# Kernel tuning notes

Hardware: AMD Instinct MI355X
Metric: run time of the kernel (lower is better)

## Reference

```python
import jax, jax.numpy as jnp
import numpy as np

EMB = 768
HEADS = 8
HEAD_DIM = EMB // HEADS  # 96


def setup_inputs() -> dict:
    key = jax.random.key(0)
    k1, k2, k3, k4, k5 = jax.random.split(key, 5)
    N, S = 2, 4096
    values = jax.random.normal(k1, (N, S, EMB), dtype=jnp.float32)
    keys = jax.random.normal(k2, (N, S, EMB), dtype=jnp.float32)
    query = jax.random.normal(k3, (N, S, EMB), dtype=jnp.float32)
    # fc_out: nn.Linear(emb_size, emb_size) -> weight [out,in], bias [out]
    bound = 1.0 / np.sqrt(EMB)
    fc_w = jax.random.uniform(k4, (EMB, EMB), dtype=jnp.float32, minval=-bound, maxval=bound)
    fc_b = jax.random.uniform(k5, (EMB,), dtype=jnp.float32, minval=-bound, maxval=bound)
    return {"values": values, "keys": keys, "query": query, "fc_w": fc_w, "fc_b": fc_b}


def reference(values, keys, query, fc_w, fc_b):
    # NOTE: original forward never uses the per-head q/k/v Linear layers;
    # it reshapes raw inputs into heads directly. We reproduce that faithfully.
    N, Sq, _ = query.shape
    # [N, S, E] -> [N, H, S, D]
    q = query.reshape(N, Sq, HEADS, HEAD_DIM).transpose(0, 2, 1, 3)
    k = keys.reshape(N, -1, HEADS, HEAD_DIM).transpose(0, 2, 1, 3)
    v = values.reshape(N, -1, HEADS, HEAD_DIM).transpose(0, 2, 1, 3)
    scale = 1.0 / np.sqrt(HEAD_DIM).astype(np.float32)
    scores = jnp.einsum('nhqd,nhkd->nhqk', q, k) * scale  # [N,H,Sq,Sk]
    p = jax.nn.softmax(scores, axis=-1)
    x = jnp.einsum('nhqk,nhkd->nhqd', p, v)  # [N,H,Sq,D]
    x = x.transpose(0, 2, 1, 3).reshape(N, Sq, EMB)
    return x @ fc_w.T + fc_b
```

## Files before the change

kernel.cpp:

```cpp
#include <hip/hip_runtime.h>
#include <hip/hip_bf16.h>

#define S_LEN 4096
#define EMB 768
#define NHEAD 8
#define HDIM 96

typedef short bf16x8 __attribute__((ext_vector_type(8)));
typedef float f32x4 __attribute__((ext_vector_type(4)));
typedef float f32x16 __attribute__((ext_vector_type(16)));

__device__ __forceinline__ short f2bf(float x) {
  union { float f; unsigned u; } v; v.f = x;
  unsigned r = v.u + 0x7fffu + ((v.u >> 16) & 1u);
  return (short)(r >> 16);
}

__device__ __forceinline__ short f2bfh(float x) {
  union { __hip_bfloat16 h; short s; } u;
  u.h = __float2bfloat16(x);
  return u.s;
}

#define GLOAD_LDS16(gp, lp)                                              \
  __builtin_amdgcn_global_load_lds(                                      \
      (const __attribute__((address_space(1))) unsigned int*)(gp),       \
      (__attribute__((address_space(3))) unsigned int*)(lp), 16, 0, 0)

__global__ __launch_bounds__(256) void prep_kernel(const float* __restrict__ K,
                                                   const float* __restrict__ W,
                                                   const float* __restrict__ V,
                                                   short* __restrict__ KVT,
                                                   short* __restrict__ Wb) {
  __shared__ short tlbuf[6656];
  int b = blockIdx.x;
  int tid = threadIdx.x;
  if (b < 288) {
    int t = b * 256 + tid;
    size_t off = (size_t)t * 8;
    float4 a = *(const float4*)(W + off);
    float4 bq = *(const float4*)(W + off + 4);
    bf16x8 r;
    r[0]=f2bf(a.x);  r[1]=f2bf(a.y);  r[2]=f2bf(a.z);  r[3]=f2bf(a.w);
    r[4]=f2bf(bq.x); r[5]=f2bf(bq.y); r[6]=f2bf(bq.z); r[7]=f2bf(bq.w);
    *(bf16x8*)(Wb + off) = r;
    return;
  }
  if (b < 1312) {
    int bb = b - 288;
    int n = bb >> 9, h = (bb >> 6) & 7, st = bb & 63;
    int s0 = st * 64;
    const float* kp = K + ((size_t)(n * S_LEN + s0)) * EMB + h * HDIM;
    #pragma unroll
    for (int k = 0; k < 6; ++k) {
      int idx = k * 256 + tid;
      int fidx = idx * 4;
      int s = fidx / 96, d = fidx % 96;
      float4 a = *(const float4*)(kp + (size_t)s * EMB + d);
      short* t4 = &tlbuf[s * 104 + d];
      t4[0] = f2bf(a.x); t4[1] = f2bf(a.y); t4[2] = f2bf(a.z); t4[3] = f2bf(a.w);
    }
    __syncthreads();
    short* KVp = KVT + ((size_t)((n * NHEAD + h) * 64 + st)) * 12288;
    #pragma unroll
    for (int i = 0; i < 3; ++i) {
      int u = i * 256 + tid;
      int c = u >> 7, rem = u & 127;
      int ksub = (rem >> 6) & 1, hi2 = (rem >> 5) & 1, l31 = rem & 31;
      int key = ksub * 32 + l31;
      int db = c * 16 + hi2 * 8;
      short4 lo = *(const short4*)&tlbuf[key * 104 + db];
      short4 hi4 = *(const short4*)&tlbuf[key * 104 + db + 4];
      bf16x8 r;
      r[0]=lo.x; r[1]=lo.y; r[2]=lo.z; r[3]=lo.w;
      r[4]=hi4.x; r[5]=hi4.y; r[6]=hi4.z; r[7]=hi4.w;
      *(bf16x8*)(KVp + (size_t)u * 8) = r;
    }
    return;
  }
  int bb = b - 1312;
  int n = bb >> 9, h = (bb >> 6) & 7, st = bb & 63;
  int s0 = st * 64;
  const float* vp = V + ((size_t)(n * S_LEN + s0)) * EMB + h * HDIM;
  #pragma unroll
  for (int k = 0; k < 6; ++k) {
    int idx = k * 256 + tid;
    int fidx = idx * 4;
    int s = fidx / 96, d = fidx % 96;
    float4 a = *(const float4*)(vp + (size_t)s * EMB + d);
    tlbuf[(d + 0) * 68 + s] = f2bf(a.x);
    tlbuf[(d + 1) * 68 + s] = f2bf(a.y);
    tlbuf[(d + 2) * 68 + s] = f2bf(a.z);
    tlbuf[(d + 3) * 68 + s] = f2bf(a.w);
  }
  __syncthreads();
  short* KVp = KVT + ((size_t)((n * NHEAD + h) * 64 + st)) * 12288 + 6144;
  #pragma unroll
  for (int i = 0; i < 3; ++i) {
    int u = i * 256 + tid;
    int slice = u / 192;
    int rem = u - slice * 192;
    int dt = rem >> 6, hi2 = (rem >> 5) & 1, d5 = rem & 31;
    int d = dt * 32 + d5;
    int kb = 16 * slice + 4 * hi2;
    short4 lo = *(const short4*)&tlbuf[d * 68 + kb];
    short4 hi4 = *(const short4*)&tlbuf[d * 68 + kb + 8];
    bf16x8 r;
    r[0]=lo.x; r[1]=lo.y; r[2]=lo.z; r[3]=lo.w;
    r[4]=hi4.x; r[5]=hi4.y; r[6]=hi4.z; r[7]=hi4.w;
    *(bf16x8*)(KVp + (size_t)u * 8) = r;
  }
}

template<int NKG>
__global__ __launch_bounds__(128, 2) void attn_kernel(const float* __restrict__ Q,
                                                      const short* __restrict__ KVT,
                                                      short* __restrict__ Xb,
                                                      float* __restrict__ Op,
                                                      float* __restrict__ lp) {
  __shared__ __align__(16) char smem[36864];
  constexpr int ITERS = S_LEN / NKG / 64;
  int L = blockIdx.x;
  int bb = L & 511;
  int kg = L >> 9;
  int h = bb & 7, j = bb >> 3;
  int n = j >> 5, qt = j & 31;
  int q0 = qt * 128;
  int tid = threadIdx.x;
  int w = tid >> 6, lane = tid & 63, l31 = lane & 31, hi = lane >> 5;

  const float kAdj = 0.14724512f;
  bf16x8 qfa[6], qfb[6];
  #pragma unroll
  for (int sub = 0; sub < 2; ++sub) {
    const float* qp = Q + ((size_t)(n * S_LEN + q0 + w * 64 + sub * 32 + l31)) * EMB
                        + h * HDIM + 8 * hi;
    #pragma unroll
    for (int c = 0; c < 6; ++c) {
      float4 a = *(const float4*)(qp + 16 * c);
      float4 bq = *(const float4*)(qp + 16 * c + 4);
      bf16x8 r;
      r[0]=f2bf(a.x*kAdj);  r[1]=f2bf(a.y*kAdj);  r[2]=f2bf(a.z*kAdj);  r[3]=f2bf(a.w*kAdj);
      r[4]=f2bf(bq.x*kAdj); r[5]=f2bf(bq.y*kAdj); r[6]=f2bf(bq.z*kAdj); r[7]=f2bf(bq.w*kAdj);
      if (sub == 0) qfa[c] = r; else qfb[c] = r;
    }
  }

  const short* gKV = KVT + ((size_t)((n * NHEAD + h) * 64 + kg * ITERS)) * 12288
                        + (size_t)(w * 6) * 512 + lane * 8;
  char* kbuf = smem;
  char* vbuf = smem + 12288;
  char* kdst = kbuf + w * 6144;
  char* vdst0 = vbuf + w * 6144;

  #pragma unroll
  for (int i = 0; i < 6; ++i) {
    GLOAD_LDS16(gKV + i * 512, kdst + i * 1024);
    GLOAD_LDS16(gKV + 6144 + i * 512, vdst0 + i * 1024);
  }
  __syncthreads();

  f32x16 oa[3], ob[3];
  #pragma unroll
  for (int dt = 0; dt < 3; ++dt) { oa[dt] = (f32x16){}; ob[dt] = (f32x16){}; }
  float tsa = 0.f, tsb = 0.f;

  int cur = 0;
  #pragma unroll 1
  for (int t = 0; t < ITERS; ++t) {
    f32x16 s0a = (f32x16){}, s1a = (f32x16){}, s0b = (f32x16){}, s1b = (f32x16){};
    __builtin_amdgcn_s_setprio(1);
    #pragma unroll
    for (int c = 0; c < 6; ++c) {
      bf16x8 kf0 = *(const bf16x8*)(kbuf + c * 2048 + lane * 16);
      bf16x8 kf1 = *(const bf16x8*)(kbuf + c * 2048 + 1024 + lane * 16);
      s0a = __builtin_amdgcn_mfma_f32_32x32x16_bf16(kf0, qfa[c], s0a, 0, 0, 0);
      s0b = __builtin_amdgcn_mfma_f32_32x32x16_bf16(kf0, qfb[c], s0b, 0, 0, 0);
      s1a = __builtin_amdgcn_mfma_f32_32x32x16_bf16(kf1, qfa[c], s1a, 0, 0, 0);
      s1b = __builtin_amdgcn_mfma_f32_32x32x16_bf16(kf1, qfb[c], s1b, 0, 0, 0);
    }
    __builtin_amdgcn_s_setprio(0);
    __syncthreads();

    if (t < ITERS - 1) {
      const short* src = gKV + (size_t)(t + 1) * 12288;
      char* vd = vbuf + (cur ^ 1) * 12288 + w * 6144;
      #pragma unroll
      for (int i = 0; i < 6; ++i) {
        GLOAD_LDS16(src + i * 512, kdst + i * 1024);
        GLOAD_LDS16(src + 6144 + i * 512, vd + i * 1024);
      }
    }

    #pragma unroll
    for (int r = 0; r < 16; ++r) s0a[r] = __builtin_amdgcn_exp2f(s0a[r]);
    #pragma unroll
    for (int r = 0; r < 16; ++r) s1a[r] = __builtin_amdgcn_exp2f(s1a[r]);
    #pragma unroll
    for (int r = 0; r < 16; ++r) s0b[r] = __builtin_amdgcn_exp2f(s0b[r]);
    #pragma unroll
    for (int r = 0; r < 16; ++r) s1b[r] = __builtin_amdgcn_exp2f(s1b[r]);
    {
      float a0 = (s0a[0]+s0a[1])+(s0a[2]+s0a[3]), a1 = (s0a[4]+s0a[5])+(s0a[6]+s0a[7]);
      float a2 = (s0a[8]+s0a[9])+(s0a[10]+s0a[11]), a3 = (s0a[12]+s0a[13])+(s0a[14]+s0a[15]);
      float b0 = (s1a[0]+s1a[1])+(s1a[2]+s1a[3]), b1 = (s1a[4]+s1a[5])+(s1a[6]+s1a[7]);
      float b2 = (s1a[8]+s1a[9])+(s1a[10]+s1a[11]), b3 = (s1a[12]+s1a[13])+(s1a[14]+s1a[15]);
      tsa += ((a0+a1)+(a2+a3)) + ((b0+b1)+(b2+b3));
      float c0 = (s0b[0]+s0b[1])+(s0b[2]+s0b[3]), c1 = (s0b[4]+s0b[5])+(s0b[6]+s0b[7]);
      float c2 = (s0b[8]+s0b[9])+(s0b[10]+s0b[11]), c3 = (s0b[12]+s0b[13])+(s0b[14]+s0b[15]);
      float d0_ = (s1b[0]+s1b[1])+(s1b[2]+s1b[3]), d1_ = (s1b[4]+s1b[5])+(s1b[6]+s1b[7]);
      float d2_ = (s1b[8]+s1b[9])+(s1b[10]+s1b[11]), d3_ = (s1b[12]+s1b[13])+(s1b[14]+s1b[15]);
      tsb += ((c0+c1)+(c2+c3)) + ((d0_+d1_)+(d2_+d3_));
    }

    const char* vbl = vbuf + cur * 12288;
    #pragma unroll
    for (int ksub = 0; ksub < 2; ++ksub) {
      const f32x16& sa = ksub ? s1a : s0a;
      const f32x16& sb = ksub ? s1b : s0b;
      #pragma unroll
      for (int ks = 0; ks < 2; ++ks) {
        unsigned a0, a1, a2, a3, b0, b1, b2, b3;
        asm("v_cvt_pk_bf16_f32 %0, %1, %2" : "=v"(a0) : "v"(sa[8*ks+0]), "v"(sa[8*ks+1]));
        asm("v_cvt_pk_bf16_f32 %0, %1, %2" : "=v"(a1) : "v"(sa[8*ks+2]), "v"(sa[8*ks+3]));
        asm("v_cvt_pk_bf16_f32 %0, %1, %2" : "=v"(a2) : "v"(sa[8*ks+4]), "v"(sa[8*ks+5]));
        asm("v_cvt_pk_bf16_f32 %0, %1, %2" : "=v"(a3) : "v"(sa[8*ks+6]), "v"(sa[8*ks+7]));
        asm("v_cvt_pk_bf16_f32 %0, %1, %2" : "=v"(b0) : "v"(sb[8*ks+0]), "v"(sb[8*ks+1]));
        asm("v_cvt_pk_bf16_f32 %0, %1, %2" : "=v"(b1) : "v"(sb[8*ks+2]), "v"(sb[8*ks+3]));
        asm("v_cvt_pk_bf16_f32 %0, %1, %2" : "=v"(b2) : "v"(sb[8*ks+4]), "v"(sb[8*ks+5]));
        asm("v_cvt_pk_bf16_f32 %0, %1, %2" : "=v"(b3) : "v"(sb[8*ks+6]), "v"(sb[8*ks+7]));
        union { unsigned u[4]; bf16x8 v; } pa, pb;
        pa.u[0] = a0; pa.u[1] = a1; pa.u[2] = a2; pa.u[3] = a3;
        pb.u[0] = b0; pb.u[1] = b1; pb.u[2] = b2; pb.u[3] = b3;
        int slice = 2 * ksub + ks;
        __builtin_amdgcn_s_setprio(1);
        #pragma unroll
        for (int dt = 0; dt < 3; ++dt) {
          bf16x8 vf = *(const bf16x8*)(vbl + (slice * 3 + dt) * 1024 + hi * 512 + l31 * 16);
          oa[dt] = __builtin_amdgcn_mfma_f32_32x32x16_bf16(pa.v, vf, oa[dt], 0, 0, 0);
          ob[dt] = __builtin_amdgcn_mfma_f32_32x32x16_bf16(pb.v, vf, ob[dt], 0, 0, 0);
        }
        __builtin_amdgcn_s_setprio(0);
      }
    }
    __syncthreads();
    cur ^= 1;
  }

  float la = tsa + __shfl_xor(tsa, 32, 64);
  float lb = tsb + __shfl_xor(tsb, 32, 64);

  if constexpr (NKG > 1) {
    float* op = Op + (size_t)L * 12288;
    #pragma unroll
    for (int p = 0; p < 4; ++p) {
      #pragma unroll
      for (int jj = 0; jj < 4; ++jj) {
        int qra = w * 64 + 8 * p + 4 * hi + jj;
        op[(size_t)qra * 96 + l31]      = oa[0][4*p+jj];
        op[(size_t)qra * 96 + 32 + l31] = oa[1][4*p+jj];
        op[(size_t)qra * 96 + 64 + l31] = oa[2][4*p+jj];
        int qrb = qra + 32;
        op[(size_t)qrb * 96 + l31]      = ob[0][4*p+jj];
        op[(size_t)qrb * 96 + 32 + l31] = ob[1][4*p+jj];
        op[(size_t)qrb * 96 + 64 + l31] = ob[2][4*p+jj];
      }
    }
    if (hi == 0) {
      lp[(size_t)L * 128 + w * 64 + l31] = la;
      lp[(size_t)L * 128 + w * 64 + 32 + l31] = lb;
    }
  } else {
    __syncthreads();
    float* bcf = (float*)smem;
    if (hi == 0) {
      bcf[w * 64 + l31] = 1.0f / la;
      bcf[w * 64 + 32 + l31] = 1.0f / lb;
    }
    __syncthreads();
    #pragma unroll
    for (int p = 0; p < 4; ++p) {
      #pragma unroll
      for (int jj = 0; jj < 4; ++jj) {
        int qr = 8 * p + 4 * hi + jj;
        float iva = bcf[w * 64 + qr];
        float ivb = bcf[w * 64 + 32 + qr];
        short* xpa = Xb + ((size_t)(n * S_LEN + q0 + w * 64 + qr)) * EMB + h * HDIM + l31;
        xpa[0]  = f2bfh(oa[0][4*p+jj] * iva);
        xpa[32] = f2bfh(oa[1][4*p+jj] * iva);
        xpa[64] = f2bfh(oa[2][4*p+jj] * iva);
        short* xpb = xpa + (size_t)32 * EMB;
        xpb[0]  = f2bfh(ob[0][4*p+jj] * ivb);
        xpb[32] = f2bfh(ob[1][4*p+jj] * ivb);
        xpb[64] = f2bfh(ob[2][4*p+jj] * ivb);
      }
    }
  }
}

__global__ __launch_bounds__(256) void combine_kernel(const float* __restrict__ Op,
                                                      const float* __restrict__ lp,
                                                      short* __restrict__ Xb,
                                                      int nkg) {
  int b = blockIdx.x;
  int h = b & 7, j = b >> 3, n = j >> 5, qt = j & 31;
  int q0 = qt * 128;
  int tid = threadIdx.x;
  #pragma unroll 1
  for (int i = 0; i < 12; ++i) {
    int idx = (i * 256 + tid) * 4;
    int qr = idx / 96, d = idx - qr * 96;
    float ax = 0.f, ay = 0.f, az = 0.f, aw = 0.f, l = 0.f;
    for (int kg = 0; kg < nkg; ++kg) {
      size_t blk = (size_t)(kg * 512 + b);
      float4 v = *(const float4*)(Op + blk * 12288 + idx);
      ax += v.x; ay += v.y; az += v.z; aw += v.w;
      l += lp[blk * 128 + qr];
    }
    float iv = 1.0f / l;
    short4 r;
    r.x = f2bfh(ax * iv); r.y = f2bfh(ay * iv);
    r.z = f2bfh(az * iv); r.w = f2bfh(aw * iv);
    *(short4*)(Xb + ((size_t)(n * S_LEN + q0 + qr)) * EMB + h * HDIM + d) = r;
  }
}

__global__ __launch_bounds__(256) void fc_kernel(const short* __restrict__ Xb,
                                                 const short* __restrict__ Wb,
                                                 const float* __restrict__ bias,
                                                 float* __restrict__ out) {
  int m0 = blockIdx.x * 64, j0 = blockIdx.y * 64;
  int tid = threadIdx.x;
  int w = tid >> 6, lane = tid & 63, lr = lane & 15, lg = lane >> 4;
  f32x4 acc[4];
  #pragma unroll
  for (int jt = 0; jt < 4; ++jt) acc[jt] = (f32x4){0.f, 0.f, 0.f, 0.f};
  const short* xp = Xb + (size_t)(m0 + w * 16 + lr) * EMB + 8 * lg;
  const short* wp = Wb + (size_t)(j0 + lr) * EMB + 8 * lg;
  #pragma unroll 1
  for (int kt = 0; kt < 24; ++kt) {
    bf16x8 a = *(const bf16x8*)(xp + kt * 32);
    #pragma unroll
    for (int jt = 0; jt < 4; ++jt) {
      bf16x8 bw = *(const bf16x8*)(wp + (size_t)(jt * 16) * EMB + kt * 32);
      acc[jt] = __builtin_amdgcn_mfma_f32_16x16x32_bf16(a, bw, acc[jt], 0, 0, 0);
    }
  }
  #pragma unroll
  for (int jt = 0; jt < 4; ++jt) {
    float bb = bias[j0 + jt * 16 + lr];
    #pragma unroll
    for (int i = 0; i < 4; ++i)
      out[(size_t)(m0 + w * 16 + 4 * lg + i) * EMB + j0 + jt * 16 + lr] = acc[jt][i] + bb;
  }
}

extern "C" void kernel_launch(void* const* d_in, const int* in_sizes, int n_in,
                              void* d_out, int out_size, void* d_ws, size_t ws_size,
                              hipStream_t stream) {
  (void)in_sizes; (void)n_in; (void)out_size;
  const float* V = (const float*)d_in[0];
  const float* K = (const float*)d_in[1];
  const float* Q = (const float*)d_in[2];
  const float* W = (const float*)d_in[3];
  const float* B = (const float*)d_in[4];
  float* out = (float*)d_out;
  short* KVT = (short*)d_ws;
  short* Wb  = KVT + 12582912;
  short* Xb  = Wb + 589824;
  size_t base_bytes = (size_t)(12582912 + 589824 + 6291456) * 2;
  size_t part_bytes = (size_t)2 * 512 * (12288 + 128) * 4;
  prep_kernel<<<2336, 256, 0, stream>>>(K, W, V, KVT, Wb);
  if (ws_size >= base_bytes + part_bytes) {
    float* Op = (float*)((char*)d_ws + base_bytes);
    float* lp = Op + (size_t)2 * 512 * 12288;
    attn_kernel<2><<<1024, 128, 0, stream>>>(Q, KVT, Xb, Op, lp);
    combine_kernel<<<512, 256, 0, stream>>>(Op, lp, Xb, 2);
  } else {
    attn_kernel<1><<<512, 128, 0, stream>>>(Q, KVT, Xb, nullptr, nullptr);
  }
  fc_kernel<<<dim3(128, 12), 256, 0, stream>>>(Xb, Wb, B, out);
}
```

Before: 213.8 us.

## Store split-K partials in bf16 and issue V prefetch before QK MMAs

Measured after the change: 210.4 us. Within noise of the previous version (-1.6%).

```diff
diff --git a/kernel.cpp b/kernel.cpp
--- a/kernel.cpp
+++ b/kernel.cpp
@@ -20,6 +20,12 @@
   union { __hip_bfloat16 h; short s; } u;
   u.h = __float2bfloat16(x);
   return u.s;
+}
+
+__device__ __forceinline__ float bf2f(short s) {
+  union { unsigned u; float f; } v;
+  v.u = ((unsigned)(unsigned short)s) << 16;
+  return v.f;
 }
 
 #define GLOAD_LDS16(gp, lp)                                              \
@@ -116,7 +122,7 @@
 __global__ __launch_bounds__(128, 2) void attn_kernel(const float* __restrict__ Q,
                                                       const short* __restrict__ KVT,
                                                       short* __restrict__ Xb,
-                                                      float* __restrict__ Op,
+                                                      short* __restrict__ Op,
                                                       float* __restrict__ lp) {
   __shared__ __align__(16) char smem[36864];
   constexpr int ITERS = S_LEN / NKG / 64;
@@ -168,6 +174,14 @@
   int cur = 0;
   #pragma unroll 1
   for (int t = 0; t < ITERS; ++t) {
+    if (t < ITERS - 1) {
+      const short* src = gKV + (size_t)(t + 1) * 12288;
+      char* vd = vbuf + (cur ^ 1) * 12288 + w * 6144;
+      #pragma unroll
+      for (int i = 0; i < 6; ++i)
+        GLOAD_LDS16(src + 6144 + i * 512, vd + i * 1024);
+    }
+
     f32x16 s0a = (f32x16){}, s1a = (f32x16){}, s0b = (f32x16){}, s1b = (f32x16){};
     __builtin_amdgcn_s_setprio(1);
     #pragma unroll
@@ -184,12 +198,9 @@
 
     if (t < ITERS - 1) {
       const short* src = gKV + (size_t)(t + 1) * 12288;
-      char* vd = vbuf + (cur ^ 1) * 12288 + w * 6144;
-      #pragma unroll
-      for (int i = 0; i < 6; ++i) {
+      #pragma unroll
+      for (int i = 0; i < 6; ++i)
         GLOAD_LDS16(src + i * 512, kdst + i * 1024);
-        GLOAD_LDS16(src + 6144 + i * 512, vd + i * 1024);
-      }
     }
 
     #pragma unroll
@@ -251,19 +262,19 @@
   float lb = tsb + __shfl_xor(tsb, 32, 64);
 
   if constexpr (NKG > 1) {
-    float* op = Op + (size_t)L * 12288;
+    short* op = Op + (size_t)L * 12288;
     #pragma unroll
     for (int p = 0; p < 4; ++p) {
       #pragma unroll
       for (int jj = 0; jj < 4; ++jj) {
         int qra = w * 64 + 8 * p + 4 * hi + jj;
-        op[(size_t)qra * 96 + l31]      = oa[0][4*p+jj];
-        op[(size_t)qra * 96 + 32 + l31] = oa[1][4*p+jj];
-        op[(size_t)qra * 96 + 64 + l31] = oa[2][4*p+jj];
+        op[(size_t)qra * 96 + l31]      = f2bfh(oa[0][4*p+jj]);
+        op[(size_t)qra * 96 + 32 + l31] = f2bfh(oa[1][4*p+jj]);
+        op[(size_t)qra * 96 + 64 + l31] = f2bfh(oa[2][4*p+jj]);
         int qrb = qra + 32;
-        op[(size_t)qrb * 96 + l31]      = ob[0][4*p+jj];
-        op[(size_t)qrb * 96 + 32 + l31] = ob[1][4*p+jj];
-        op[(size_t)qrb * 96 + 64 + l31] = ob[2][4*p+jj];
+        op[(size_t)qrb * 96 + l31]      = f2bfh(ob[0][4*p+jj]);
+        op[(size_t)qrb * 96 + 32 + l31] = f2bfh(ob[1][4*p+jj]);
+        op[(size_t)qrb * 96 + 64 + l31] = f2bfh(ob[2][4*p+jj]);
       }
     }
     if (hi == 0) {
@@ -298,7 +309,7 @@
   }
 }
 
-__global__ __launch_bounds__(256) void combine_kernel(const float* __restrict__ Op,
+__global__ __launch_bounds__(256) void combine_kernel(const short* __restrict__ Op,
                                                       const float* __restrict__ lp,
                                                       short* __restrict__ Xb,
                                                       int nkg) {
@@ -307,21 +318,23 @@
   int q0 = qt * 128;
   int tid = threadIdx.x;
   #pragma unroll 1
-  for (int i = 0; i < 12; ++i) {
-    int idx = (i * 256 + tid) * 4;
+  for (int i = 0; i < 6; ++i) {
+    int idx = (i * 256 + tid) * 8;
     int qr = idx / 96, d = idx - qr * 96;
-    float ax = 0.f, ay = 0.f, az = 0.f, aw = 0.f, l = 0.f;
+    float acc[8] = {0.f, 0.f, 0.f, 0.f, 0.f, 0.f, 0.f, 0.f};
+    float l = 0.f;
     for (int kg = 0; kg < nkg; ++kg) {
       size_t blk = (size_t)(kg * 512 + b);
-      float4 v = *(const float4*)(Op + blk * 12288 + idx);
-      ax += v.x; ay += v.y; az += v.z; aw += v.w;
+      bf16x8 v = *(const bf16x8*)(Op + blk * 12288 + idx);
+      #pragma unroll
+      for (int e = 0; e < 8; ++e) acc[e] += bf2f(v[e]);
       l += lp[blk * 128 + qr];
     }
     float iv = 1.0f / l;
-    short4 r;
-    r.x = f2bfh(ax * iv); r.y = f2bfh(ay * iv);
-    r.z = f2bfh(az * iv); r.w = f2bfh(aw * iv);
-    *(short4*)(Xb + ((size_t)(n * S_LEN + q0 + qr)) * EMB + h * HDIM + d) = r;
+    bf16x8 r;
+    #pragma unroll
+    for (int e = 0; e < 8; ++e) r[e] = f2bfh(acc[e] * iv);
+    *(bf16x8*)(Xb + ((size_t)(n * S_LEN + q0 + qr)) * EMB + h * HDIM + d) = r;
   }
 }
 
@@ -369,11 +382,11 @@
   short* Wb  = KVT + 12582912;
   short* Xb  = Wb + 589824;
   size_t base_bytes = (size_t)(12582912 + 589824 + 6291456) * 2;
-  size_t part_bytes = (size_t)2 * 512 * (12288 + 128) * 4;
+  size_t part_bytes = (size_t)2 * 512 * 12288 * 2 + (size_t)2 * 512 * 128 * 4;
   prep_kernel<<<2336, 256, 0, stream>>>(K, W, V, KVT, Wb);
   if (ws_size >= base_bytes + part_bytes) {
-    float* Op = (float*)((char*)d_ws + base_bytes);
-    float* lp = Op + (size_t)2 * 512 * 12288;
+    short* Op = (short*)((char*)d_ws + base_bytes);
+    float* lp = (float*)(Op + (size_t)2 * 512 * 12288);
     attn_kernel<2><<<1024, 128, 0, stream>>>(Q, KVT, Xb, Op, lp);
     combine_kernel<<<512, 256, 0, stream>>>(Op, lp, Xb, 2);
   } else {
```
